# Performance work log

Measured on AMD Instinct MI355X. Metric: run time of the kernel, lower is better.

## Reference

```python
import jax, jax.numpy as jnp
import numpy as np

D_MODEL = 1024


def setup_inputs() -> dict:
    key = jax.random.key(0)
    ks = jax.random.split(key, 7)
    d = D_MODEL
    x = jax.random.normal(ks[0], (4, 2048, d), dtype=jnp.float32)
    scale = 1.0 / np.sqrt(d)
    Wq = jax.random.normal(ks[1], (d, d), dtype=jnp.float32) * scale
    bq = jax.random.normal(ks[2], (d,), dtype=jnp.float32) * 0.01
    Wk = jax.random.normal(ks[3], (d, d), dtype=jnp.float32) * scale
    bk = jax.random.normal(ks[4], (d,), dtype=jnp.float32) * 0.01
    Wo = jax.random.normal(ks[5], (d, 1), dtype=jnp.float32) * scale
    bo = jax.random.normal(ks[6], (1,), dtype=jnp.float32) * 0.01
    return {"x": x, "Wq": Wq, "bq": bq, "Wk": Wk, "bk": bk, "Wo": Wo, "bo": bo}


def reference(x, Wq, bq, Wk, bk, Wo, bo):
    # x: [B, N, d]
    Q = x @ Wq + bq                      # [B, N, d]
    K = x @ Wk + bk                      # [B, N, d]
    scale = x.shape[-1] ** (-0.5)
    content_logits = jnp.einsum('bnd,bmd->bnm', Q, K) * scale  # [B, N, N]
    s = (x @ Wo + bo)[..., 0]            # [B, N]
    # ordering_bias[b, i, j] = tanh(s[b, j] - s[b, i]) * 5
    ordering_bias = jnp.tanh(s[:, None, :] - s[:, :, None]) * 5.0
    return content_logits + ordering_bias
```

## Files before the change

### kernel.cpp

```cpp
#include <hip/hip_runtime.h>
#include <math.h>

#define D_MODEL 1024
#define SEQ 2048
#define SCALE 0.03125f

using bf16x8 = __attribute__((ext_vector_type(8))) short;
using f32x4  = __attribute__((ext_vector_type(4))) float;

__device__ __forceinline__ unsigned short f2bf(float f) {
  union { float f; unsigned int u; } v; v.f = f;
  return (unsigned short)((v.u + 0x7fffu + ((v.u >> 16) & 1u)) >> 16);
}

__device__ __forceinline__ void async_cp16(const void* g, void* l) {
  __builtin_amdgcn_global_load_lds(
      (const __attribute__((address_space(1))) void*)g,
      (__attribute__((address_space(3))) void*)l, 16, 0, 0);
}

__device__ __forceinline__ const unsigned short* stage_ptr(
    const unsigned short* base, int row0, int ld, int tid) {
  const int r0 = tid >> 2;
  const int s0 = ((tid & 3) ^ ((r0 >> 1) & 3)) * 8;
  return base + (size_t)(row0 + r0) * ld + s0;
}

__device__ __forceinline__ void gemm_core(
    const unsigned short* __restrict__ gA, const unsigned short* __restrict__ gB,
    int lda, int ldb, unsigned short* As, unsigned short* Bs, int tid,
    f32x4 acc[4][4]) {
  const int lane = tid & 63, w = tid >> 6;
  const int wm = w >> 1, wn = w & 1;
  const int l16 = lane & 15, quad = lane >> 4;

  async_cp16(gA,            As + tid * 8);
  async_cp16(gA + 64 * lda, As + 2048 + tid * 8);
  async_cp16(gB,            Bs + tid * 8);
  async_cp16(gB + 64 * ldb, Bs + 2048 + tid * 8);
  __syncthreads();

  #pragma unroll 2
  for (int kk = 0; kk < 32; ++kk) {
    const int cur = (kk & 1) * 4096;
    const int nxt = 4096 - cur;
    if (kk < 31) {
      const unsigned short* a = gA + (kk + 1) * 32;
      const unsigned short* b = gB + (kk + 1) * 32;
      async_cp16(a,            As + nxt + tid * 8);
      async_cp16(a + 64 * lda, As + nxt + 2048 + tid * 8);
      async_cp16(b,            Bs + nxt + tid * 8);
      async_cp16(b + 64 * ldb, Bs + nxt + 2048 + tid * 8);
    }
    bf16x8 afr[4], bfr[4];
    #pragma unroll
    for (int mt = 0; mt < 4; mt++) {
      const int R = wm * 64 + mt * 16 + l16;
      afr[mt] = *(const bf16x8*)(As + cur + (R * 4 + (quad ^ ((R >> 1) & 3))) * 8);
    }
    #pragma unroll
    for (int nt = 0; nt < 4; nt++) {
      const int R = wn * 64 + nt * 16 + l16;
      bfr[nt] = *(const bf16x8*)(Bs + cur + (R * 4 + (quad ^ ((R >> 1) & 3))) * 8);
    }
    #pragma unroll
    for (int mt = 0; mt < 4; mt++)
      #pragma unroll
      for (int nt = 0; nt < 4; nt++)
        acc[mt][nt] = __builtin_amdgcn_mfma_f32_16x16x32_bf16(
            afr[mt], bfr[nt], acc[mt][nt], 0, 0, 0);
    __syncthreads();
  }
}

__device__ __forceinline__ void store_c_bf16(f32x4 acc[4][4],
                                             unsigned short* C, int ldc,
                                             int m0, int n0, int tid) {
  const int lane = tid & 63, w = tid >> 6;
  const int wm = w >> 1, wn = w & 1;
  const int l16 = lane & 15, quad = lane >> 4;
  #pragma unroll
  for (int mt = 0; mt < 4; mt++) {
    #pragma unroll
    for (int r = 0; r < 4; r++) {
      const int row = m0 + wm * 64 + mt * 16 + quad * 4 + r;
      unsigned short* cp = C + (size_t)row * ldc + n0 + wn * 64 + l16;
      #pragma unroll
      for (int nt = 0; nt < 4; nt++) cp[nt * 16] = f2bf(acc[mt][nt][r]);
    }
  }
}

__global__ __launch_bounds__(256) void wcvt_kernel(
    const float* __restrict__ Wq, const float* __restrict__ Wk,
    const float* __restrict__ bq, const float* __restrict__ bk,
    unsigned short* __restrict__ Wqb, unsigned short* __restrict__ Wkb,
    float* __restrict__ u, float* __restrict__ v, float* __restrict__ sc) {
  const int blk = blockIdx.x, tid = threadIdx.x;
  __shared__ float red[4];
  float p;
  if (blk < 2048) {
    const bool isq = blk < 1024;
    const int row = blk & 1023;
    const float* W = isq ? Wq : Wk;
    const float* bias = isq ? bk : bq;
    const float4 wv = ((const float4*)(W + (size_t)row * D_MODEL))[tid];
    const float4 bv = ((const float4*)bias)[tid];
    ushort4 o;
    o.x = f2bf(wv.x); o.y = f2bf(wv.y); o.z = f2bf(wv.z); o.w = f2bf(wv.w);
    ((ushort4*)((isq ? Wqb : Wkb) + (size_t)row * D_MODEL))[tid] = o;
    p = wv.x * bv.x + wv.y * bv.y + wv.z * bv.z + wv.w * bv.w;
    #pragma unroll
    for (int off = 32; off > 0; off >>= 1) p += __shfl_down(p, off, 64);
    if ((tid & 63) == 0) red[tid >> 6] = p;
    __syncthreads();
    if (tid == 0) (isq ? u : v)[row] = red[0] + red[1] + red[2] + red[3];
  } else {
    const float4 a = ((const float4*)bq)[tid];
    const float4 b = ((const float4*)bk)[tid];
    p = a.x * b.x + a.y * b.y + a.z * b.z + a.w * b.w;
    #pragma unroll
    for (int off = 32; off > 0; off >>= 1) p += __shfl_down(p, off, 64);
    if ((tid & 63) == 0) red[tid >> 6] = p;
    __syncthreads();
    if (tid == 0) sc[0] = SCALE * (red[0] + red[1] + red[2] + red[3]);
  }
}

__global__ __launch_bounds__(256) void prep_x_kernel(
    const float* __restrict__ x, const float* __restrict__ Wo,
    const float* __restrict__ bo, const float* __restrict__ u,
    const float* __restrict__ v, const float* __restrict__ sc,
    unsigned short* __restrict__ xb, float* __restrict__ tb,
    float* __restrict__ aa, float* __restrict__ bb) {
  const int m = blockIdx.x, tid = threadIdx.x;
  const float4 xv = ((const float4*)(x + (size_t)m * D_MODEL))[tid];
  const float4 wv = ((const float4*)Wo)[tid];
  const float4 uv = ((const float4*)u)[tid];
  const float4 vv = ((const float4*)v)[tid];
  ushort4 o;
  o.x = f2bf(xv.x); o.y = f2bf(xv.y); o.z = f2bf(xv.z); o.w = f2bf(xv.w);
  ((ushort4*)(xb + (size_t)m * D_MODEL))[tid] = o;
  float p0 = xv.x * wv.x + xv.y * wv.y + xv.z * wv.z + xv.w * wv.w;
  float p1 = xv.x * uv.x + xv.y * uv.y + xv.z * uv.z + xv.w * uv.w;
  float p2 = xv.x * vv.x + xv.y * vv.y + xv.z * vv.z + xv.w * vv.w;
  #pragma unroll
  for (int off = 32; off > 0; off >>= 1) {
    p0 += __shfl_down(p0, off, 64);
    p1 += __shfl_down(p1, off, 64);
    p2 += __shfl_down(p2, off, 64);
  }
  __shared__ float red[3][4];
  if ((tid & 63) == 0) {
    red[0][tid >> 6] = p0; red[1][tid >> 6] = p1; red[2][tid >> 6] = p2;
  }
  __syncthreads();
  if (tid == 0) {
    tb[m] = tanhf(red[0][0] + red[0][1] + red[0][2] + red[0][3] + bo[0]);
    aa[m] = SCALE * (red[1][0] + red[1][1] + red[1][2] + red[1][3]) + sc[0];
    bb[m] = SCALE * (red[2][0] + red[2][1] + red[2][2] + red[2][3]);
  }
}

__global__ __launch_bounds__(256, 3) void wmm_kernel(
    const unsigned short* __restrict__ Wkb,
    const unsigned short* __restrict__ Wqb, unsigned short* __restrict__ Mt) {
  const int m0 = blockIdx.x * 128, n0 = blockIdx.y * 128;
  __shared__ unsigned short As[2 * 4096], Bs[2 * 4096];
  const int tid = threadIdx.x;
  f32x4 acc[4][4];
  #pragma unroll
  for (int i = 0; i < 4; i++)
    #pragma unroll
    for (int j = 0; j < 4; j++) acc[i][j] = f32x4{0.f, 0.f, 0.f, 0.f};
  gemm_core(stage_ptr(Wkb, m0, D_MODEL, tid), stage_ptr(Wqb, n0, D_MODEL, tid),
            D_MODEL, D_MODEL, As, Bs, tid, acc);
  store_c_bf16(acc, Mt, D_MODEL, m0, n0, tid);
}

__global__ __launch_bounds__(256, 3) void zgen_kernel(
    const unsigned short* __restrict__ xb,
    const unsigned short* __restrict__ Mt, unsigned short* __restrict__ Zb) {
  const int m0 = blockIdx.x * 128, n0 = blockIdx.y * 128;
  __shared__ unsigned short As[2 * 4096], Bs[2 * 4096];
  const int tid = threadIdx.x;
  f32x4 acc[4][4];
  #pragma unroll
  for (int i = 0; i < 4; i++)
    #pragma unroll
    for (int j = 0; j < 4; j++) acc[i][j] = f32x4{0.f, 0.f, 0.f, 0.f};
  gemm_core(stage_ptr(xb, m0, D_MODEL, tid), stage_ptr(Mt, n0, D_MODEL, tid),
            D_MODEL, D_MODEL, As, Bs, tid, acc);
  store_c_bf16(acc, Zb, D_MODEL, m0, n0, tid);
}

__global__ __launch_bounds__(256, 3) void zxt_kernel(
    const unsigned short* __restrict__ Zb, const unsigned short* __restrict__ xb,
    const float* __restrict__ tb, const float* __restrict__ aa,
    const float* __restrict__ bb, float* __restrict__ out) {
  const int b = blockIdx.z;
  const int i0 = blockIdx.x * 128, j0 = blockIdx.y * 128;
  __shared__ unsigned short As[2 * 4096], Bs[2 * 4096];
  __shared__ float tsi[128], tsj[128], tsa[128], tsb[128];
  const int tid = threadIdx.x;
  if (tid < 128) {
    tsi[tid] = tb[b * SEQ + i0 + tid];
    tsa[tid] = aa[b * SEQ + i0 + tid];
  } else {
    tsj[tid - 128] = tb[b * SEQ + j0 + tid - 128];
    tsb[tid - 128] = bb[b * SEQ + j0 + tid - 128];
  }
  f32x4 acc[4][4];
  #pragma unroll
  for (int i = 0; i < 4; i++)
    #pragma unroll
    for (int j = 0; j < 4; j++) acc[i][j] = f32x4{0.f, 0.f, 0.f, 0.f};
  const unsigned short* A = Zb + (size_t)b * SEQ * D_MODEL;
  const unsigned short* Bt = xb + (size_t)b * SEQ * D_MODEL;
  gemm_core(stage_ptr(A, i0, D_MODEL, tid), stage_ptr(Bt, j0, D_MODEL, tid),
            D_MODEL, D_MODEL, As, Bs, tid, acc);

  const int lane = tid & 63, w = tid >> 6;
  const int wm = w >> 1, wn = w & 1;
  const int l16 = lane & 15, quad = lane >> 4;
  float tj[4], bj[4];
  #pragma unroll
  for (int nt = 0; nt < 4; nt++) {
    tj[nt] = tsj[wn * 64 + nt * 16 + l16];
    bj[nt] = tsb[wn * 64 + nt * 16 + l16];
  }
  #pragma unroll
  for (int mt = 0; mt < 4; mt++) {
    #pragma unroll
    for (int r = 0; r < 4; r++) {
      const int il = wm * 64 + mt * 16 + quad * 4 + r;
      const float ti = tsi[il];
      const float ai = tsa[il];
      float* cp = out + ((size_t)(b * SEQ + i0 + il)) * SEQ + j0 + wn * 64 + l16;
      #pragma unroll
      for (int nt = 0; nt < 4; nt++) {
        const float num = tj[nt] - ti;
        const float den = fmaf(-tj[nt], ti, 1.0f);
        const float obias = 5.0f * num * __builtin_amdgcn_rcpf(den);
        cp[nt * 16] = SCALE * acc[mt][nt][r] + ai + bj[nt] + obias;
      }
    }
  }
}

extern "C" void kernel_launch(void* const* d_in, const int* in_sizes, int n_in,
                              void* d_out, int out_size, void* d_ws, size_t ws_size,
                              hipStream_t stream) {
  const float* x  = (const float*)d_in[0];
  const float* Wq = (const float*)d_in[1];
  const float* bq = (const float*)d_in[2];
  const float* Wk = (const float*)d_in[3];
  const float* bk = (const float*)d_in[4];
  const float* Wo = (const float*)d_in[5];
  const float* bo = (const float*)d_in[6];
  float* out = (float*)d_out;

  char* ws = (char*)d_ws;
  unsigned short* xb  = (unsigned short*)(ws);
  unsigned short* Zb  = (unsigned short*)(ws + (16ull << 20));
  unsigned short* Wqb = (unsigned short*)(ws + (32ull << 20));
  unsigned short* Wkb = (unsigned short*)(ws + (34ull << 20));
  unsigned short* Mt  = (unsigned short*)(ws + (36ull << 20));
  float* tb = (float*)(ws + (38ull << 20));
  float* aa = (float*)(ws + (38ull << 20) + (32ull << 10));
  float* bb = (float*)(ws + (38ull << 20) + (64ull << 10));
  float* u  = (float*)(ws + (38ull << 20) + (96ull << 10));
  float* v  = (float*)(ws + (38ull << 20) + (100ull << 10));
  float* sc = (float*)(ws + (38ull << 20) + (104ull << 10));

  wcvt_kernel<<<2049, 256, 0, stream>>>(Wq, Wk, bq, bk, Wqb, Wkb, u, v, sc);
  prep_x_kernel<<<8192, 256, 0, stream>>>(x, Wo, bo, u, v, sc, xb, tb, aa, bb);
  wmm_kernel<<<dim3(8, 8), 256, 0, stream>>>(Wkb, Wqb, Mt);
  zgen_kernel<<<dim3(64, 8), 256, 0, stream>>>(xb, Mt, Zb);
  zxt_kernel<<<dim3(16, 16, 4), 256, 0, stream>>>(Zb, xb, tb, aa, bb, out);
}
```

Measured before the change: 194.7 us.

## Switch GEMMs to 256x128 tiles with triple-buffered BK=64 pipeline

```diff
diff --git a/kernel.cpp b/kernel.cpp
--- a/kernel.cpp
+++ b/kernel.cpp
@@ -19,64 +19,118 @@
       (__attribute__((address_space(3))) void*)l, 16, 0, 0);
 }
 
-__device__ __forceinline__ const unsigned short* stage_ptr(
-    const unsigned short* base, int row0, int ld, int tid) {
-  const int r0 = tid >> 2;
-  const int s0 = ((tid & 3) ^ ((r0 >> 1) & 3)) * 8;
-  return base + (size_t)(row0 + r0) * ld + s0;
-}
-
-__device__ __forceinline__ void gemm_core(
-    const unsigned short* __restrict__ gA, const unsigned short* __restrict__ gB,
-    int lda, int ldb, unsigned short* As, unsigned short* Bs, int tid,
-    f32x4 acc[4][4]) {
-  const int lane = tid & 63, w = tid >> 6;
-  const int wm = w >> 1, wn = w & 1;
-  const int l16 = lane & 15, quad = lane >> 4;
-
-  async_cp16(gA,            As + tid * 8);
-  async_cp16(gA + 64 * lda, As + 2048 + tid * 8);
-  async_cp16(gB,            Bs + tid * 8);
-  async_cp16(gB + 64 * ldb, Bs + 2048 + tid * 8);
-  __syncthreads();
-
-  #pragma unroll 2
-  for (int kk = 0; kk < 32; ++kk) {
-    const int cur = (kk & 1) * 4096;
-    const int nxt = 4096 - cur;
-    if (kk < 31) {
-      const unsigned short* a = gA + (kk + 1) * 32;
-      const unsigned short* b = gB + (kk + 1) * 32;
-      async_cp16(a,            As + nxt + tid * 8);
-      async_cp16(a + 64 * lda, As + nxt + 2048 + tid * 8);
-      async_cp16(b,            Bs + nxt + tid * 8);
-      async_cp16(b + 64 * ldb, Bs + nxt + 2048 + tid * 8);
-    }
-    bf16x8 afr[4], bfr[4];
-    #pragma unroll
-    for (int mt = 0; mt < 4; mt++) {
-      const int R = wm * 64 + mt * 16 + l16;
-      afr[mt] = *(const bf16x8*)(As + cur + (R * 4 + (quad ^ ((R >> 1) & 3))) * 8);
-    }
-    #pragma unroll
-    for (int nt = 0; nt < 4; nt++) {
-      const int R = wn * 64 + nt * 16 + l16;
-      bfr[nt] = *(const bf16x8*)(Bs + cur + (R * 4 + (quad ^ ((R >> 1) & 3))) * 8);
-    }
-    #pragma unroll
-    for (int mt = 0; mt < 4; mt++)
+
+#define ASLOT 16384
+#define BSLOT 8192
+
+__device__ __forceinline__ void stage_tile(const unsigned short* sA,
+                                           const unsigned short* sB,
+                                           unsigned short* As,
+                                           unsigned short* Bs, int s, int kt,
+                                           int t) {
+  const unsigned short* a = sA + kt * 64;
+  const unsigned short* b = sB + kt * 64;
+  unsigned short* da = As + s * ASLOT + t * 8;
+  unsigned short* db = Bs + s * BSLOT + t * 8;
+  async_cp16(a, da);
+  async_cp16(a + 64 * D_MODEL, da + 4096);
+  async_cp16(a + 128 * D_MODEL, da + 8192);
+  async_cp16(a + 192 * D_MODEL, da + 12288);
+  async_cp16(b, db);
+  async_cp16(b + 64 * D_MODEL, db + 4096);
+}
+
+template <bool STG>
+__device__ __forceinline__ void tile_body(unsigned short* As, unsigned short* Bs,
+                                          int slot, int s2, int ktN,
+                                          const unsigned short* sA,
+                                          const unsigned short* sB, int t,
+                                          int aoff, int boff, int ka0, int ka1,
+                                          f32x4 (&acc)[4][4]) {
+  const unsigned short* Ab = As + slot * ASLOT + aoff;
+  const unsigned short* Bb = Bs + slot * BSLOT + boff;
+  bf16x8 bfr[4][2], afr[2][2], afr2[2][2];
+  #pragma unroll
+  for (int nt = 0; nt < 4; nt++) {
+    bfr[nt][0] = *(const bf16x8*)(Bb + nt * 1024 + ka0);
+    bfr[nt][1] = *(const bf16x8*)(Bb + nt * 1024 + ka1);
+  }
+  #pragma unroll
+  for (int mt = 0; mt < 2; mt++) {
+    afr[mt][0] = *(const bf16x8*)(Ab + mt * 1024 + ka0);
+    afr[mt][1] = *(const bf16x8*)(Ab + mt * 1024 + ka1);
+  }
+  if (STG) stage_tile(sA, sB, As, Bs, s2, ktN, t);
+  __builtin_amdgcn_s_setprio(1);
+  #pragma unroll
+  for (int ks = 0; ks < 2; ks++)
+    #pragma unroll
+    for (int mt = 0; mt < 2; mt++)
       #pragma unroll
       for (int nt = 0; nt < 4; nt++)
         acc[mt][nt] = __builtin_amdgcn_mfma_f32_16x16x32_bf16(
-            afr[mt], bfr[nt], acc[mt][nt], 0, 0, 0);
-    __syncthreads();
-  }
-}
-
-__device__ __forceinline__ void store_c_bf16(f32x4 acc[4][4],
-                                             unsigned short* C, int ldc,
-                                             int m0, int n0, int tid) {
-  const int lane = tid & 63, w = tid >> 6;
+            afr[mt][ks], bfr[nt][ks], acc[mt][nt], 0, 0, 0);
+  __builtin_amdgcn_s_setprio(0);
+  #pragma unroll
+  for (int mt = 0; mt < 2; mt++) {
+    afr2[mt][0] = *(const bf16x8*)(Ab + (2 + mt) * 1024 + ka0);
+    afr2[mt][1] = *(const bf16x8*)(Ab + (2 + mt) * 1024 + ka1);
+  }
+  __builtin_amdgcn_s_setprio(1);
+  #pragma unroll
+  for (int ks = 0; ks < 2; ks++)
+    #pragma unroll
+    for (int mt = 0; mt < 2; mt++)
+      #pragma unroll
+      for (int nt = 0; nt < 4; nt++)
+        acc[2 + mt][nt] = __builtin_amdgcn_mfma_f32_16x16x32_bf16(
+            afr2[mt][ks], bfr[nt][ks], acc[2 + mt][nt], 0, 0, 0);
+  __builtin_amdgcn_s_setprio(0);
+}
+
+#define PIPE_SYNC(N)                                      \
+  asm volatile("s_waitcnt vmcnt(" #N ")" ::: "memory");   \
+  __builtin_amdgcn_s_barrier();                           \
+  asm volatile("" ::: "memory")
+
+__device__ __forceinline__ void gemm256x128(const unsigned short* gA,
+                                            const unsigned short* gB,
+                                            unsigned short* As,
+                                            unsigned short* Bs, int t,
+                                            f32x4 (&acc)[4][4]) {
+  const int srow = t >> 3;
+  const int schk = (t & 7) ^ (srow & 7);
+  const unsigned short* sA = gA + srow * D_MODEL + schk * 8;
+  const unsigned short* sB = gB + srow * D_MODEL + schk * 8;
+  const int lane = t & 63, w = t >> 6;
+  const int wm = w >> 1, wn = w & 1;
+  const int l16 = lane & 15, quad = lane >> 4, x7 = l16 & 7;
+  const int aoff = (wm * 64 + l16) * 64;
+  const int boff = (wn * 64 + l16) * 64;
+  const int ka0 = (quad ^ x7) * 8;
+  const int ka1 = ((4 | quad) ^ x7) * 8;
+
+  stage_tile(sA, sB, As, Bs, 0, 0, t);
+  stage_tile(sA, sB, As, Bs, 1, 1, t);
+
+  int slot = 0, s2 = 2;
+  for (int kt = 0; kt < 14; ++kt) {
+    PIPE_SYNC(6);
+    tile_body<true>(As, Bs, slot, s2, kt + 2, sA, sB, t, aoff, boff, ka0, ka1,
+                    acc);
+    slot = (slot == 2) ? 0 : slot + 1;
+    s2 = (s2 == 2) ? 0 : s2 + 1;
+  }
+  PIPE_SYNC(6);
+  tile_body<false>(As, Bs, 2, 0, 0, sA, sB, t, aoff, boff, ka0, ka1, acc);
+  PIPE_SYNC(0);
+  tile_body<false>(As, Bs, 0, 0, 0, sA, sB, t, aoff, boff, ka0, ka1, acc);
+}
+
+__device__ __forceinline__ void store_bf16_256x128(f32x4 (&acc)[4][4],
+                                                   unsigned short* C, int ldc,
+                                                   int m0, int n0, int t) {
+  const int lane = t & 63, w = t >> 6;
   const int wm = w >> 1, wn = w & 1;
   const int l16 = lane & 15, quad = lane >> 4;
   #pragma unroll
@@ -162,72 +216,72 @@
   }
 }
 
-__global__ __launch_bounds__(256, 3) void wmm_kernel(
+__global__ __launch_bounds__(512, 2) void wmm_kernel(
     const unsigned short* __restrict__ Wkb,
     const unsigned short* __restrict__ Wqb, unsigned short* __restrict__ Mt) {
-  const int m0 = blockIdx.x * 128, n0 = blockIdx.y * 128;
-  __shared__ unsigned short As[2 * 4096], Bs[2 * 4096];
-  const int tid = threadIdx.x;
+  __shared__ unsigned short As[3 * ASLOT], Bs[3 * BSLOT];
+  const int n0 = blockIdx.x * 128, m0 = blockIdx.y * 256;
+  const int t = threadIdx.x;
   f32x4 acc[4][4];
   #pragma unroll
   for (int i = 0; i < 4; i++)
     #pragma unroll
     for (int j = 0; j < 4; j++) acc[i][j] = f32x4{0.f, 0.f, 0.f, 0.f};
-  gemm_core(stage_ptr(Wkb, m0, D_MODEL, tid), stage_ptr(Wqb, n0, D_MODEL, tid),
-            D_MODEL, D_MODEL, As, Bs, tid, acc);
-  store_c_bf16(acc, Mt, D_MODEL, m0, n0, tid);
-}
-
-__global__ __launch_bounds__(256, 3) void zgen_kernel(
+  gemm256x128(Wkb + (size_t)m0 * D_MODEL, Wqb + (size_t)n0 * D_MODEL, As, Bs, t,
+              acc);
+  store_bf16_256x128(acc, Mt, D_MODEL, m0, n0, t);
+}
+
+__global__ __launch_bounds__(512, 2) void zgen_kernel(
     const unsigned short* __restrict__ xb,
     const unsigned short* __restrict__ Mt, unsigned short* __restrict__ Zb) {
-  const int m0 = blockIdx.x * 128, n0 = blockIdx.y * 128;
-  __shared__ unsigned short As[2 * 4096], Bs[2 * 4096];
-  const int tid = threadIdx.x;
+  __shared__ unsigned short As[3 * ASLOT], Bs[3 * BSLOT];
+  const int n0 = blockIdx.x * 128, m0 = blockIdx.y * 256;
+  const int t = threadIdx.x;
   f32x4 acc[4][4];
   #pragma unroll
   for (int i = 0; i < 4; i++)
     #pragma unroll
     for (int j = 0; j < 4; j++) acc[i][j] = f32x4{0.f, 0.f, 0.f, 0.f};
-  gemm_core(stage_ptr(xb, m0, D_MODEL, tid), stage_ptr(Mt, n0, D_MODEL, tid),
-            D_MODEL, D_MODEL, As, Bs, tid, acc);
-  store_c_bf16(acc, Zb, D_MODEL, m0, n0, tid);
-}
-
-__global__ __launch_bounds__(256, 3) void zxt_kernel(
+  gemm256x128(xb + (size_t)m0 * D_MODEL, Mt + (size_t)n0 * D_MODEL, As, Bs, t,
+              acc);
+  store_bf16_256x128(acc, Zb, D_MODEL, m0, n0, t);
+}
+
+__global__ __launch_bounds__(512, 2) void zxt_kernel(
     const unsigned short* __restrict__ Zb, const unsigned short* __restrict__ xb,
     const float* __restrict__ tb, const float* __restrict__ aa,
     const float* __restrict__ bb, float* __restrict__ out) {
+  __shared__ unsigned short As[3 * ASLOT], Bs[3 * BSLOT];
+  __shared__ float tsi[256], tsa[256], tsj[128], tsb2[128];
   const int b = blockIdx.z;
-  const int i0 = blockIdx.x * 128, j0 = blockIdx.y * 128;
-  __shared__ unsigned short As[2 * 4096], Bs[2 * 4096];
-  __shared__ float tsi[128], tsj[128], tsa[128], tsb[128];
-  const int tid = threadIdx.x;
-  if (tid < 128) {
-    tsi[tid] = tb[b * SEQ + i0 + tid];
-    tsa[tid] = aa[b * SEQ + i0 + tid];
-  } else {
-    tsj[tid - 128] = tb[b * SEQ + j0 + tid - 128];
-    tsb[tid - 128] = bb[b * SEQ + j0 + tid - 128];
-  }
+  const int j0 = blockIdx.x * 128, i0 = blockIdx.y * 256;
+  const int t = threadIdx.x;
   f32x4 acc[4][4];
   #pragma unroll
   for (int i = 0; i < 4; i++)
     #pragma unroll
     for (int j = 0; j < 4; j++) acc[i][j] = f32x4{0.f, 0.f, 0.f, 0.f};
-  const unsigned short* A = Zb + (size_t)b * SEQ * D_MODEL;
-  const unsigned short* Bt = xb + (size_t)b * SEQ * D_MODEL;
-  gemm_core(stage_ptr(A, i0, D_MODEL, tid), stage_ptr(Bt, j0, D_MODEL, tid),
-            D_MODEL, D_MODEL, As, Bs, tid, acc);
-
-  const int lane = tid & 63, w = tid >> 6;
+  gemm256x128(Zb + ((size_t)b * SEQ + i0) * D_MODEL,
+              xb + ((size_t)b * SEQ + j0) * D_MODEL, As, Bs, t, acc);
+
+  if (t < 256) {
+    tsi[t] = tb[b * SEQ + i0 + t];
+    tsa[t] = aa[b * SEQ + i0 + t];
+  } else if (t < 384) {
+    tsj[t - 256] = tb[b * SEQ + j0 + t - 256];
+    tsb2[t - 256] = bb[b * SEQ + j0 + t - 256];
+  }
+  __syncthreads();
+
+  const int lane = t & 63, w = t >> 6;
   const int wm = w >> 1, wn = w & 1;
   const int l16 = lane & 15, quad = lane >> 4;
   float tj[4], bj[4];
   #pragma unroll
   for (int nt = 0; nt < 4; nt++) {
     tj[nt] = tsj[wn * 64 + nt * 16 + l16];
-    bj[nt] = tsb[wn * 64 + nt * 16 + l16];
+    bj[nt] = tsb2[wn * 64 + nt * 16 + l16];
   }
   #pragma unroll
   for (int mt = 0; mt < 4; mt++) {
@@ -236,7 +290,8 @@
       const int il = wm * 64 + mt * 16 + quad * 4 + r;
       const float ti = tsi[il];
       const float ai = tsa[il];
-      float* cp = out + ((size_t)(b * SEQ + i0 + il)) * SEQ + j0 + wn * 64 + l16;
+      float* cp =
+          out + ((size_t)(b * SEQ + i0 + il)) * SEQ + j0 + wn * 64 + l16;
       #pragma unroll
       for (int nt = 0; nt < 4; nt++) {
         const float num = tj[nt] - ti;
@@ -249,8 +304,8 @@
 }
 
 extern "C" void kernel_launch(void* const* d_in, const int* in_sizes, int n_in,
-                              void* d_out, int out_size, void* d_ws, size_t ws_size,
-                              hipStream_t stream) {
+                              void* d_out, int out_size, void* d_ws,
+                              size_t ws_size, hipStream_t stream) {
   const float* x  = (const float*)d_in[0];
   const float* Wq = (const float*)d_in[1];
   const float* bq = (const float*)d_in[2];
@@ -275,7 +330,7 @@
 
   wcvt_kernel<<<2049, 256, 0, stream>>>(Wq, Wk, bq, bk, Wqb, Wkb, u, v, sc);
   prep_x_kernel<<<8192, 256, 0, stream>>>(x, Wo, bo, u, v, sc, xb, tb, aa, bb);
-  wmm_kernel<<<dim3(8, 8), 256, 0, stream>>>(Wkb, Wqb, Mt);
-  zgen_kernel<<<dim3(64, 8), 256, 0, stream>>>(xb, Mt, Zb);
-  zxt_kernel<<<dim3(16, 16, 4), 256, 0, stream>>>(Zb, xb, tb, aa, bb, out);
-}
+  wmm_kernel<<<dim3(8, 4), 512, 0, stream>>>(Wkb, Wqb, Mt);
+  zgen_kernel<<<dim3(8, 32), 512, 0, stream>>>(xb, Mt, Zb);
+  zxt_kernel<<<dim3(16, 8, 4), 512, 0, stream>>>(Zb, xb, tb, aa, bb, out);
+}
```

Result: slower. 198.7 us (+2.1%).

## Rewrite batched Z·xᵀ GEMM with 256x256 tiles and 8-phase async pipeline

Applied to the files above, without the earlier changes.

```diff
diff --git a/kernel.cpp b/kernel.cpp
--- a/kernel.cpp
+++ b/kernel.cpp
@@ -194,63 +194,146 @@
   store_c_bf16(acc, Zb, D_MODEL, m0, n0, tid);
 }
 
-__global__ __launch_bounds__(256, 3) void zxt_kernel(
+
+#define STAGE2(S, D) { async_cp16((S), (D)); \
+                       async_cp16((S) + 64 * D_MODEL, (D) + 4096); }
+
+#define PHASE(Q, AB, BB, LOADB, STG, VM) {                                   \
+    bf16x8 afr[2][2];                                                        \
+    if (LOADB) {                                                             \
+      _Pragma("unroll") for (int nt = 0; nt < 4; nt++) {                     \
+        bfr[nt][0] = *(const bf16x8*)((BB) + brow + nt * 1024 + c0);         \
+        bfr[nt][1] = *(const bf16x8*)((BB) + brow + nt * 1024 + c1);         \
+      }                                                                      \
+    }                                                                        \
+    _Pragma("unroll") for (int mt = 0; mt < 2; mt++) {                       \
+      afr[mt][0] = *(const bf16x8*)((AB) + arow + (Q)*2048 + mt*1024 + c0);  \
+      afr[mt][1] = *(const bf16x8*)((AB) + arow + (Q)*2048 + mt*1024 + c1);  \
+    }                                                                        \
+    STG;                                                                     \
+    if ((VM) == 6) asm volatile("s_waitcnt vmcnt(6)" ::: "memory");          \
+    if ((VM) == 0) asm volatile("s_waitcnt vmcnt(0)" ::: "memory");          \
+    __builtin_amdgcn_s_barrier();                                            \
+    asm volatile("s_waitcnt lgkmcnt(0)" ::: "memory");                       \
+    __builtin_amdgcn_s_setprio(1);                                           \
+    _Pragma("unroll") for (int ks = 0; ks < 2; ks++)                         \
+      _Pragma("unroll") for (int mt = 0; mt < 2; mt++)                       \
+        _Pragma("unroll") for (int nt = 0; nt < 4; nt++)                     \
+          acc[(Q)*2 + mt][nt] = __builtin_amdgcn_mfma_f32_16x16x32_bf16(     \
+              afr[mt][ks], bfr[nt][ks], acc[(Q)*2 + mt][nt], 0, 0, 0);       \
+    __builtin_amdgcn_s_setprio(0);                                           \
+    __builtin_amdgcn_s_barrier();                                            \
+  }
+
+#define NOSTAGE ((void)0)
+
+__global__ __launch_bounds__(512, 2) void zxt_kernel(
     const unsigned short* __restrict__ Zb, const unsigned short* __restrict__ xb,
     const float* __restrict__ tb, const float* __restrict__ aa,
     const float* __restrict__ bb, float* __restrict__ out) {
+  __shared__ unsigned short As[32768], Bs[32768];
+  __shared__ float tsi[256], tsa[256], tsj[256], tsb2[256];
   const int b = blockIdx.z;
-  const int i0 = blockIdx.x * 128, j0 = blockIdx.y * 128;
-  __shared__ unsigned short As[2 * 4096], Bs[2 * 4096];
-  __shared__ float tsi[128], tsj[128], tsa[128], tsb[128];
-  const int tid = threadIdx.x;
-  if (tid < 128) {
-    tsi[tid] = tb[b * SEQ + i0 + tid];
-    tsa[tid] = aa[b * SEQ + i0 + tid];
+  const int j0 = blockIdx.x * 256, i0 = blockIdx.y * 256;
+  const int t = threadIdx.x;
+  const int lane = t & 63, w = t >> 6;
+  const int wm = w >> 2, wn = w & 3;
+  const int l16 = lane & 15, quad = lane >> 4, x7 = l16 & 7;
+  const int c0 = (quad ^ x7) * 8, c1 = ((4 | quad) ^ x7) * 8;
+  const int arow = l16 * 64;
+  const int brow = ((wn & 1) * 64 + l16) * 64;
+
+  const unsigned short* A0 = As + wm * 8192;
+  const unsigned short* A1 = As + 16384 + wm * 8192;
+  const unsigned short* B0 = Bs + (wn >> 1) * 8192;
+  const unsigned short* B1 = Bs + 16384 + (wn >> 1) * 8192;
+
+  const int r0 = t >> 3;
+  const int sc_ = (t & 7) ^ (r0 & 7);
+  const unsigned short* sA =
+      Zb + ((size_t)b * SEQ + i0 + r0) * D_MODEL + sc_ * 8;
+  const unsigned short* sB =
+      xb + ((size_t)b * SEQ + j0 + r0) * D_MODEL + sc_ * 8;
+  unsigned short* dA = As + t * 8;
+  unsigned short* dB = Bs + t * 8;
+
+  f32x4 acc[8][4];
+  #pragma unroll
+  for (int i = 0; i < 8; i++)
+    #pragma unroll
+    for (int j = 0; j < 4; j++) acc[i][j] = f32x4{0.f, 0.f, 0.f, 0.f};
+  bf16x8 bfr[4][2];
+
+  STAGE2(sB,                       dB);
+  STAGE2(sB + 128 * D_MODEL,       dB + 8192);
+  STAGE2(sA,                       dA);
+  STAGE2(sA + 128 * D_MODEL,       dA + 8192);
+  STAGE2(sB + 64,                  dB + 16384);
+  STAGE2(sB + 128 * D_MODEL + 64,  dB + 16384 + 8192);
+  STAGE2(sA + 64,                  dA + 16384);
+  asm volatile("s_waitcnt vmcnt(6)" ::: "memory");
+  __builtin_amdgcn_s_barrier();
+
+  for (int i = 0; i < 7; ++i) {
+    const int k1o = (2 * i + 1) * 64;
+    const int k2o = (2 * i + 2) * 64;
+    const int k3o = (2 * i + 3) * 64;
+    PHASE(0, A0, B0, 1, STAGE2(sA + 128 * D_MODEL + k1o, dA + 16384 + 8192), -1);
+    PHASE(1, A0, B0, 0, STAGE2(sB + k2o, dB), -1);
+    PHASE(2, A0, B0, 0, STAGE2(sB + 128 * D_MODEL + k2o, dB + 8192), -1);
+    PHASE(3, A0, B0, 0, STAGE2(sA + k2o, dA), 6);
+    PHASE(0, A1, B1, 1, STAGE2(sA + 128 * D_MODEL + k2o, dA + 8192), -1);
+    PHASE(1, A1, B1, 0, STAGE2(sB + k3o, dB + 16384), -1);
+    PHASE(2, A1, B1, 0, STAGE2(sB + 128 * D_MODEL + k3o, dB + 16384 + 8192), -1);
+    PHASE(3, A1, B1, 0, STAGE2(sA + k3o, dA + 16384), 6);
+  }
+  PHASE(0, A0, B0, 1, STAGE2(sA + 128 * D_MODEL + 15 * 64, dA + 16384 + 8192), -1);
+  PHASE(1, A0, B0, 0, NOSTAGE, -1);
+  PHASE(2, A0, B0, 0, NOSTAGE, -1);
+  PHASE(3, A0, B0, 0, NOSTAGE, 0);
+  PHASE(0, A1, B1, 1, NOSTAGE, -1);
+  PHASE(1, A1, B1, 0, NOSTAGE, -1);
+  PHASE(2, A1, B1, 0, NOSTAGE, -1);
+  PHASE(3, A1, B1, 0, NOSTAGE, -1);
+
+  if (t < 256) {
+    tsi[t] = tb[b * SEQ + i0 + t];
+    tsa[t] = aa[b * SEQ + i0 + t];
   } else {
-    tsj[tid - 128] = tb[b * SEQ + j0 + tid - 128];
-    tsb[tid - 128] = bb[b * SEQ + j0 + tid - 128];
-  }
-  f32x4 acc[4][4];
-  #pragma unroll
-  for (int i = 0; i < 4; i++)
-    #pragma unroll
-    for (int j = 0; j < 4; j++) acc[i][j] = f32x4{0.f, 0.f, 0.f, 0.f};
-  const unsigned short* A = Zb + (size_t)b * SEQ * D_MODEL;
-  const unsigned short* Bt = xb + (size_t)b * SEQ * D_MODEL;
-  gemm_core(stage_ptr(A, i0, D_MODEL, tid), stage_ptr(Bt, j0, D_MODEL, tid),
-            D_MODEL, D_MODEL, As, Bs, tid, acc);
-
-  const int lane = tid & 63, w = tid >> 6;
-  const int wm = w >> 1, wn = w & 1;
-  const int l16 = lane & 15, quad = lane >> 4;
+    tsj[t - 256] = tb[b * SEQ + j0 + t - 256];
+    tsb2[t - 256] = bb[b * SEQ + j0 + t - 256];
+  }
+  __syncthreads();
+
   float tj[4], bj[4];
   #pragma unroll
   for (int nt = 0; nt < 4; nt++) {
     tj[nt] = tsj[wn * 64 + nt * 16 + l16];
-    bj[nt] = tsb[wn * 64 + nt * 16 + l16];
-  }
-  #pragma unroll
-  for (int mt = 0; mt < 4; mt++) {
+    bj[nt] = tsb2[wn * 64 + nt * 16 + l16];
+  }
+  #pragma unroll
+  for (int m8 = 0; m8 < 8; m8++) {
     #pragma unroll
     for (int r = 0; r < 4; r++) {
-      const int il = wm * 64 + mt * 16 + quad * 4 + r;
+      const int il = wm * 128 + (m8 >> 1) * 32 + (m8 & 1) * 16 + quad * 4 + r;
       const float ti = tsi[il];
       const float ai = tsa[il];
-      float* cp = out + ((size_t)(b * SEQ + i0 + il)) * SEQ + j0 + wn * 64 + l16;
+      float* cp =
+          out + ((size_t)(b * SEQ + i0 + il)) * SEQ + j0 + wn * 64 + l16;
       #pragma unroll
       for (int nt = 0; nt < 4; nt++) {
         const float num = tj[nt] - ti;
         const float den = fmaf(-tj[nt], ti, 1.0f);
         const float obias = 5.0f * num * __builtin_amdgcn_rcpf(den);
-        cp[nt * 16] = SCALE * acc[mt][nt][r] + ai + bj[nt] + obias;
+        cp[nt * 16] = SCALE * acc[m8][nt][r] + ai + bj[nt] + obias;
       }
     }
   }
 }
 
 extern "C" void kernel_launch(void* const* d_in, const int* in_sizes, int n_in,
-                              void* d_out, int out_size, void* d_ws, size_t ws_size,
-                              hipStream_t stream) {
+                              void* d_out, int out_size, void* d_ws,
+                              size_t ws_size, hipStream_t stream) {
   const float* x  = (const float*)d_in[0];
   const float* Wq = (const float*)d_in[1];
   const float* bq = (const float*)d_in[2];
@@ -277,5 +360,5 @@
   prep_x_kernel<<<8192, 256, 0, stream>>>(x, Wo, bo, u, v, sc, xb, tb, aa, bb);
   wmm_kernel<<<dim3(8, 8), 256, 0, stream>>>(Wkb, Wqb, Mt);
   zgen_kernel<<<dim3(64, 8), 256, 0, stream>>>(xb, Mt, Zb);
-  zxt_kernel<<<dim3(16, 16, 4), 256, 0, stream>>>(Zb, xb, tb, aa, bb, out);
-}
+  zxt_kernel<<<dim3(8, 8, 4), 512, 0, stream>>>(Zb, xb, tb, aa, bb, out);
+}
```

Result: no change. 197.1 us (+1.2%).

## Double K-tile depth to 64 and remap zxt blocks for XCD-local L2 reuse

Applied to the files above, without the earlier changes.

```diff
diff --git a/kernel.cpp b/kernel.cpp
--- a/kernel.cpp
+++ b/kernel.cpp
@@ -19,56 +19,65 @@
       (__attribute__((address_space(3))) void*)l, 16, 0, 0);
 }
 
-__device__ __forceinline__ const unsigned short* stage_ptr(
-    const unsigned short* base, int row0, int ld, int tid) {
-  const int r0 = tid >> 2;
-  const int s0 = ((tid & 3) ^ ((r0 >> 1) & 3)) * 8;
-  return base + (size_t)(row0 + r0) * ld + s0;
-}
-
-__device__ __forceinline__ void gemm_core(
-    const unsigned short* __restrict__ gA, const unsigned short* __restrict__ gB,
-    int lda, int ldb, unsigned short* As, unsigned short* Bs, int tid,
-    f32x4 acc[4][4]) {
-  const int lane = tid & 63, w = tid >> 6;
+
+__device__ __forceinline__ const unsigned short* sptr(
+    const unsigned short* base, int row0, int t) {
+  const int rr = t >> 3;
+  const int ck = (t & 7) ^ (rr & 7);
+  return base + (size_t)(row0 + rr) * D_MODEL + ck * 8;
+}
+
+#define STG8(KT, BUF) {                                                    \
+    const unsigned short* a_ = sA + (KT) * 64;                             \
+    const unsigned short* b_ = sB + (KT) * 64;                             \
+    unsigned short* da_ = As + (BUF) * 8192 + t * 8;                       \
+    unsigned short* db_ = Bs + (BUF) * 8192 + t * 8;                       \
+    async_cp16(a_,                 da_);                                   \
+    async_cp16(a_ + 32 * D_MODEL,  da_ + 2048);                            \
+    async_cp16(a_ + 64 * D_MODEL,  da_ + 4096);                            \
+    async_cp16(a_ + 96 * D_MODEL,  da_ + 6144);                            \
+    async_cp16(b_,                 db_);                                   \
+    async_cp16(b_ + 32 * D_MODEL,  db_ + 2048);                            \
+    async_cp16(b_ + 64 * D_MODEL,  db_ + 4096);                            \
+    async_cp16(b_ + 96 * D_MODEL,  db_ + 6144);                            \
+  }
+
+__device__ __forceinline__ void gemm128_bk64(
+    const unsigned short* sA, const unsigned short* sB,
+    unsigned short* As, unsigned short* Bs, int t, f32x4 acc[4][4]) {
+  const int lane = t & 63, w = t >> 6;
   const int wm = w >> 1, wn = w & 1;
-  const int l16 = lane & 15, quad = lane >> 4;
-
-  async_cp16(gA,            As + tid * 8);
-  async_cp16(gA + 64 * lda, As + 2048 + tid * 8);
-  async_cp16(gB,            Bs + tid * 8);
-  async_cp16(gB + 64 * ldb, Bs + 2048 + tid * 8);
+  const int l16 = lane & 15, quad = lane >> 4, x7 = l16 & 7;
+  const int c0 = (quad ^ x7) * 8, c1 = ((4 | quad) ^ x7) * 8;
+
+  STG8(0, 0);
   __syncthreads();
 
   #pragma unroll 2
-  for (int kk = 0; kk < 32; ++kk) {
-    const int cur = (kk & 1) * 4096;
-    const int nxt = 4096 - cur;
-    if (kk < 31) {
-      const unsigned short* a = gA + (kk + 1) * 32;
-      const unsigned short* b = gB + (kk + 1) * 32;
-      async_cp16(a,            As + nxt + tid * 8);
-      async_cp16(a + 64 * lda, As + nxt + 2048 + tid * 8);
-      async_cp16(b,            Bs + nxt + tid * 8);
-      async_cp16(b + 64 * ldb, Bs + nxt + 2048 + tid * 8);
-    }
-    bf16x8 afr[4], bfr[4];
+  for (int kk = 0; kk < 16; ++kk) {
+    const int cur = (kk & 1) * 8192;
+    if (kk < 15) STG8(kk + 1, (kk & 1) ^ 1);
+    bf16x8 afr[4][2], bfr[4][2];
     #pragma unroll
     for (int mt = 0; mt < 4; mt++) {
-      const int R = wm * 64 + mt * 16 + l16;
-      afr[mt] = *(const bf16x8*)(As + cur + (R * 4 + (quad ^ ((R >> 1) & 3))) * 8);
+      const int base = cur + (wm * 64 + mt * 16 + l16) * 64;
+      afr[mt][0] = *(const bf16x8*)(As + base + c0);
+      afr[mt][1] = *(const bf16x8*)(As + base + c1);
     }
     #pragma unroll
     for (int nt = 0; nt < 4; nt++) {
-      const int R = wn * 64 + nt * 16 + l16;
-      bfr[nt] = *(const bf16x8*)(Bs + cur + (R * 4 + (quad ^ ((R >> 1) & 3))) * 8);
-    }
-    #pragma unroll
-    for (int mt = 0; mt < 4; mt++)
+      const int base = cur + (wn * 64 + nt * 16 + l16) * 64;
+      bfr[nt][0] = *(const bf16x8*)(Bs + base + c0);
+      bfr[nt][1] = *(const bf16x8*)(Bs + base + c1);
+    }
+    #pragma unroll
+    for (int ks = 0; ks < 2; ks++)
       #pragma unroll
-      for (int nt = 0; nt < 4; nt++)
-        acc[mt][nt] = __builtin_amdgcn_mfma_f32_16x16x32_bf16(
-            afr[mt], bfr[nt], acc[mt][nt], 0, 0, 0);
+      for (int mt = 0; mt < 4; mt++)
+        #pragma unroll
+        for (int nt = 0; nt < 4; nt++)
+          acc[mt][nt] = __builtin_amdgcn_mfma_f32_16x16x32_bf16(
+              afr[mt][ks], bfr[nt][ks], acc[mt][nt], 0, 0, 0);
     __syncthreads();
   }
 }
@@ -162,95 +171,97 @@
   }
 }
 
-__global__ __launch_bounds__(256, 3) void wmm_kernel(
+__global__ __launch_bounds__(256, 2) void wmm_kernel(
     const unsigned short* __restrict__ Wkb,
     const unsigned short* __restrict__ Wqb, unsigned short* __restrict__ Mt) {
   const int m0 = blockIdx.x * 128, n0 = blockIdx.y * 128;
-  __shared__ unsigned short As[2 * 4096], Bs[2 * 4096];
-  const int tid = threadIdx.x;
+  __shared__ unsigned short As[2 * 8192], Bs[2 * 8192];
+  const int t = threadIdx.x;
   f32x4 acc[4][4];
   #pragma unroll
   for (int i = 0; i < 4; i++)
     #pragma unroll
     for (int j = 0; j < 4; j++) acc[i][j] = f32x4{0.f, 0.f, 0.f, 0.f};
-  gemm_core(stage_ptr(Wkb, m0, D_MODEL, tid), stage_ptr(Wqb, n0, D_MODEL, tid),
-            D_MODEL, D_MODEL, As, Bs, tid, acc);
-  store_c_bf16(acc, Mt, D_MODEL, m0, n0, tid);
-}
-
-__global__ __launch_bounds__(256, 3) void zgen_kernel(
+  gemm128_bk64(sptr(Wkb, m0, t), sptr(Wqb, n0, t), As, Bs, t, acc);
+  store_c_bf16(acc, Mt, D_MODEL, m0, n0, t);
+}
+
+__global__ __launch_bounds__(256, 2) void zgen_kernel(
     const unsigned short* __restrict__ xb,
     const unsigned short* __restrict__ Mt, unsigned short* __restrict__ Zb) {
   const int m0 = blockIdx.x * 128, n0 = blockIdx.y * 128;
-  __shared__ unsigned short As[2 * 4096], Bs[2 * 4096];
-  const int tid = threadIdx.x;
+  __shared__ unsigned short As[2 * 8192], Bs[2 * 8192];
+  const int t = threadIdx.x;
   f32x4 acc[4][4];
   #pragma unroll
   for (int i = 0; i < 4; i++)
     #pragma unroll
     for (int j = 0; j < 4; j++) acc[i][j] = f32x4{0.f, 0.f, 0.f, 0.f};
-  gemm_core(stage_ptr(xb, m0, D_MODEL, tid), stage_ptr(Mt, n0, D_MODEL, tid),
-            D_MODEL, D_MODEL, As, Bs, tid, acc);
-  store_c_bf16(acc, Zb, D_MODEL, m0, n0, tid);
-}
-
-__global__ __launch_bounds__(256, 3) void zxt_kernel(
+  gemm128_bk64(sptr(xb, m0, t), sptr(Mt, n0, t), As, Bs, t, acc);
+  store_c_bf16(acc, Zb, D_MODEL, m0, n0, t);
+}
+
+__global__ __launch_bounds__(256, 2) void zxt_kernel(
     const unsigned short* __restrict__ Zb, const unsigned short* __restrict__ xb,
     const float* __restrict__ tb, const float* __restrict__ aa,
     const float* __restrict__ bb, float* __restrict__ out) {
-  const int b = blockIdx.z;
-  const int i0 = blockIdx.x * 128, j0 = blockIdx.y * 128;
-  __shared__ unsigned short As[2 * 4096], Bs[2 * 4096];
-  __shared__ float tsi[128], tsj[128], tsa[128], tsb[128];
-  const int tid = threadIdx.x;
-  if (tid < 128) {
-    tsi[tid] = tb[b * SEQ + i0 + tid];
-    tsa[tid] = aa[b * SEQ + i0 + tid];
+  __shared__ unsigned short As[2 * 8192], Bs[2 * 8192];
+  __shared__ float tsi[128], tsa[128], tsj[128], tsb2[128];
+  const int n = blockIdx.z * 256 + blockIdx.y * 16 + blockIdx.x;
+  const int xcd = n & 7, q = n >> 3;
+  const int b = q >> 5, r = q & 31;
+  const int i0 = ((xcd >> 1) * 4 + (r >> 3)) * 128;
+  const int j0 = ((xcd & 1) * 8 + (r & 7)) * 128;
+  const int t = threadIdx.x;
+
+  if (t < 128) {
+    tsi[t] = tb[b * SEQ + i0 + t];
+    tsa[t] = aa[b * SEQ + i0 + t];
   } else {
-    tsj[tid - 128] = tb[b * SEQ + j0 + tid - 128];
-    tsb[tid - 128] = bb[b * SEQ + j0 + tid - 128];
-  }
+    tsj[t - 128] = tb[b * SEQ + j0 + t - 128];
+    tsb2[t - 128] = bb[b * SEQ + j0 + t - 128];
+  }
+
   f32x4 acc[4][4];
   #pragma unroll
   for (int i = 0; i < 4; i++)
     #pragma unroll
     for (int j = 0; j < 4; j++) acc[i][j] = f32x4{0.f, 0.f, 0.f, 0.f};
-  const unsigned short* A = Zb + (size_t)b * SEQ * D_MODEL;
-  const unsigned short* Bt = xb + (size_t)b * SEQ * D_MODEL;
-  gemm_core(stage_ptr(A, i0, D_MODEL, tid), stage_ptr(Bt, j0, D_MODEL, tid),
-            D_MODEL, D_MODEL, As, Bs, tid, acc);
-
-  const int lane = tid & 63, w = tid >> 6;
+  gemm128_bk64(sptr(Zb + (size_t)b * SEQ * D_MODEL, i0, t),
+               sptr(xb + (size_t)b * SEQ * D_MODEL, j0, t), As, Bs, t, acc);
+
+  const int lane = t & 63, w = t >> 6;
   const int wm = w >> 1, wn = w & 1;
   const int l16 = lane & 15, quad = lane >> 4;
   float tj[4], bj[4];
   #pragma unroll
   for (int nt = 0; nt < 4; nt++) {
     tj[nt] = tsj[wn * 64 + nt * 16 + l16];
-    bj[nt] = tsb[wn * 64 + nt * 16 + l16];
+    bj[nt] = tsb2[wn * 64 + nt * 16 + l16];
   }
   #pragma unroll
   for (int mt = 0; mt < 4; mt++) {
     #pragma unroll
-    for (int r = 0; r < 4; r++) {
-      const int il = wm * 64 + mt * 16 + quad * 4 + r;
+    for (int rr = 0; rr < 4; rr++) {
+      const int il = wm * 64 + mt * 16 + quad * 4 + rr;
       const float ti = tsi[il];
       const float ai = tsa[il];
-      float* cp = out + ((size_t)(b * SEQ + i0 + il)) * SEQ + j0 + wn * 64 + l16;
+      float* cp =
+          out + ((size_t)(b * SEQ + i0 + il)) * SEQ + j0 + wn * 64 + l16;
       #pragma unroll
       for (int nt = 0; nt < 4; nt++) {
         const float num = tj[nt] - ti;
         const float den = fmaf(-tj[nt], ti, 1.0f);
         const float obias = 5.0f * num * __builtin_amdgcn_rcpf(den);
-        cp[nt * 16] = SCALE * acc[mt][nt][r] + ai + bj[nt] + obias;
+        cp[nt * 16] = SCALE * acc[mt][nt][rr] + ai + bj[nt] + obias;
       }
     }
   }
 }
 
 extern "C" void kernel_launch(void* const* d_in, const int* in_sizes, int n_in,
-                              void* d_out, int out_size, void* d_ws, size_t ws_size,
-                              hipStream_t stream) {
+                              void* d_out, int out_size, void* d_ws,
+                              size_t ws_size, hipStream_t stream) {
   const float* x  = (const float*)d_in[0];
   const float* Wq = (const float*)d_in[1];
   const float* bq = (const float*)d_in[2];
```

Measured after the change: 182.7 us. 6.2% less time.
